# Kernel optimization log

Measured on AMD Instinct MI355X. Metric: run time of the kernel, lower is better.

## Reference

```python
import jax, jax.numpy as jnp
import numpy as np

LN_EPS = 1e-5
NORM_EPS = 1e-12


def channel_layernorm(x, w, b):
    # LayerNorm over channel dim of NCHW tensor (torch permutes to NHWC; equivalent)
    mu = x.mean(axis=1, keepdims=True)
    var = x.var(axis=1, keepdims=True)
    xn = (x - mu) / jnp.sqrt(var + LN_EPS)
    return xn * w[None, :, None, None] + b[None, :, None, None]


def pconv(x, w):
    # 1x1 pointwise conv, w: (out_ch, in_ch)
    return jnp.einsum('bchw,oc->bohw', x, w)


def dwconv3(x, w):
    # depthwise 3x3, padding 1; w: (ch, 1, 3, 3)
    return jax.lax.conv_general_dilated(
        x, w, window_strides=(1, 1), padding='SAME',
        feature_group_count=x.shape[1],
        dimension_numbers=('NCHW', 'OIHW', 'NCHW'))


def l2norm(x):
    n = jnp.sqrt(jnp.sum(x * x, axis=-1, keepdims=True))
    return x / jnp.maximum(n, NORM_EPS)


def setup_inputs() -> dict:
    key = jax.random.key(0)
    ks = jax.random.split(key, 8)
    B, C, H, W = 4, 128, 128, 128
    NH, G = 8, 2

    def w(k, shape, fan_in):
        return jax.random.normal(k, shape, dtype=jnp.float32) * (fan_in ** -0.5)

    return {
        'x': jax.random.normal(ks[0], (B, C, H, W), dtype=jnp.float32),
        'ln1_w': jnp.ones((C,), jnp.float32),
        'ln1_b': jnp.zeros((C,), jnp.float32),
        'temperature': jnp.ones((NH, 1, 1), jnp.float32),
        'qkv_p_w': w(ks[1], (3 * C, C), C),
        'qkv_d_w': w(ks[2], (3 * C, 1, 3, 3), 9),
        'proj_w': w(ks[3], (C, C), C),
        'ln2_w': jnp.ones((C,), jnp.float32),
        'ln2_b': jnp.zeros((C,), jnp.float32),
        'g1_w': w(ks[4], (2 * G * C, C), C),
        'gd_w': w(ks[5], (2 * G * C, 1, 3, 3), 9),
        'g2_w': w(ks[6], (C, G * C), G * C),
        'num_heads': NH,
    }


def reference(x, ln1_w, ln1_b, temperature, qkv_p_w, qkv_d_w, proj_w,
              ln2_w, ln2_b, g1_w, gd_w, g2_w, num_heads):
    b, c, h, w_ = x.shape
    d = c // num_heads

    # --- MDTA branch ---
    y = channel_layernorm(x, ln1_w, ln1_b)
    qkv = dwconv3(pconv(y, qkv_p_w), qkv_d_w)  # (b, 3c, h, w)
    q, k, v = jnp.split(qkv, 3, axis=1)
    q = l2norm(q.reshape(b, num_heads, d, h * w_))
    k = l2norm(k.reshape(b, num_heads, d, h * w_))
    v = v.reshape(b, num_heads, d, h * w_)
    # transposed (channel) attention: (b, heads, d, d)
    attn = jnp.einsum('bhdn,bhen->bhde', q, k) * temperature[None]
    attn = jax.nn.softmax(attn, axis=-1)
    out = jnp.einsum('bhde,bhen->bhdn', attn, v).reshape(b, c, h, w_)
    x = x + pconv(out, proj_w)

    # --- GDFN branch ---
    y = channel_layernorm(x, ln2_w, ln2_b)
    hdn = dwconv3(pconv(y, g1_w), gd_w)  # (b, 2*gamma*c, h, w)
    x1, x2 = jnp.split(hdn, 2, axis=1)
    g = jax.nn.gelu(x1, approximate=False) * x2
    x = x + pconv(g, g2_w)
    return x
```

## Files before the change

kernel.cpp:

```cpp
#include <hip/hip_runtime.h>
#include <cstdint>
#include <cstddef>

typedef float f32x4 __attribute__((ext_vector_type(4)));
typedef __bf16 bf16x8 __attribute__((ext_vector_type(8)));

__device__ __forceinline__ float b2f(unsigned short u) {
    union { unsigned int i; float f; } z; z.i = ((unsigned int)u) << 16; return z.f;
}
__device__ __forceinline__ unsigned short f2b(float f) {
    union { float f; unsigned int i; } z; z.f = f;
    unsigned int x = z.i;
    return (unsigned short)((x + 0x7FFFu + ((x >> 16) & 1u)) >> 16);
}

static constexpr int C = 128;
static constexpr int NP = 16384;
static constexpr int NH = 8;

struct Ptr11 { const float* p[11]; };
__constant__ int kWN[11]   = {128, 128, 8, 49152, 3456, 16384, 128, 128, 65536, 4608, 32768};
__constant__ int kWOff[11] = {0, 128, 256, 272, 49424, 52880, 69264, 69392, 69520, 135056, 139664};
static constexpr int kWTotal = 172432;

__global__ __launch_bounds__(256)
void cvt_w_kernel(Ptr11 P, unsigned short* __restrict__ dst)
{
    int seg = blockIdx.y;
    int n = kWN[seg];
    int i = blockIdx.x * 256 + threadIdx.x;
    if (i >= n) return;
    dst[kWOff[seg] + i] = f2b(P.p[seg][i]);
}

__device__ __forceinline__ void dw8(const unsigned short* base, int y, int xi,
                                    const float* wr, float* o)
{
    uint4 rv0 = uint4{0,0,0,0}, rv1, rv2 = uint4{0,0,0,0};
    if (y > 0)   rv0 = *(const uint4*)(base - 128);
    rv1 = *(const uint4*)(base);
    if (y < 127) rv2 = *(const uint4*)(base + 128);
    uint4 rows[3] = {rv0, rv1, rv2};
    #pragma unroll
    for (int j = 0; j < 8; ++j) o[j] = 0.f;
    #pragma unroll
    for (int r = 0; r < 3; ++r) {
        union { uint4 v; unsigned short u[8]; } cv; cv.v = rows[r];
        int lh = __shfl_up((int)cv.u[7], 1, 16);
        int rh = __shfl_down((int)cv.u[0], 1, 16);
        float p[10];
        p[0] = (xi > 0)   ? b2f((unsigned short)lh) : 0.f;
        p[9] = (xi < 120) ? b2f((unsigned short)rh) : 0.f;
        #pragma unroll
        for (int j = 0; j < 8; ++j) p[j + 1] = b2f(cv.u[j]);
        #pragma unroll
        for (int j = 0; j < 8; ++j)
            o[j] += wr[r * 3] * p[j] + wr[r * 3 + 1] * p[j + 1] + wr[r * 3 + 2] * p[j + 2];
    }
}

template <int COUT>
__device__ __forceinline__ void gemm_core_tr(
    const unsigned short* BsT,
    const unsigned short* __restrict__ W,
    unsigned short* __restrict__ OutB,
    int n0, int tid)
{
    const int lane = tid & 63;
    const int wid  = tid >> 6;
    const int ln16 = lane & 15, quad = lane >> 4;
    const int wy = wid >> 1, wx = wid & 1;
    const char* bs = (const char*)BsT;
    const int swz = (ln16 & 7) << 4;
    int rbase[4];
    #pragma unroll
    for (int nt = 0; nt < 4; ++nt) {
        int n = wx * 64 + nt * 16 + ln16;
        rbase[nt] = n * 256 + quad * 16;
    }

    for (int cc = 0; cc < COUT / 128; ++cc) {
        const int m0 = cc * 128;
        f32x4 acc[4][4];
        #pragma unroll
        for (int i = 0; i < 4; ++i)
            #pragma unroll
            for (int j = 0; j < 4; ++j) acc[i][j] = f32x4{0.f, 0.f, 0.f, 0.f};

        #pragma unroll
        for (int k0 = 0; k0 < 128; k0 += 32) {
            bf16x8 afr[4], bfr[4];
            #pragma unroll
            for (int mt = 0; mt < 4; ++mt) {
                int m = m0 + wy * 64 + mt * 16 + ln16;
                uint4 v = *(const uint4*)(W + (size_t)m * 128 + k0 + quad * 8);
                afr[mt] = *(bf16x8*)&v;
            }
            #pragma unroll
            for (int nt = 0; nt < 4; ++nt) {
                uint4 v = *(const uint4*)(bs + ((rbase[nt] + k0 * 2) ^ swz));
                bfr[nt] = *(bf16x8*)&v;
            }
            #pragma unroll
            for (int mt = 0; mt < 4; ++mt)
                #pragma unroll
                for (int nt = 0; nt < 4; ++nt)
                    acc[mt][nt] = __builtin_amdgcn_mfma_f32_16x16x32_bf16(
                        afr[mt], bfr[nt], acc[mt][nt], 0, 0, 0);
        }
        #pragma unroll
        for (int mt = 0; mt < 4; ++mt)
            #pragma unroll
            for (int nt = 0; nt < 4; ++nt) {
                int co0 = m0 + wy * 64 + mt * 16 + quad * 4;
                int n = n0 + wx * 64 + nt * 16 + ln16;
                #pragma unroll
                for (int r = 0; r < 4; ++r)
                    OutB[(size_t)(co0 + r) * NP + n] = f2b(acc[mt][nt][r]);
            }
    }
}

template <int COUT>
__global__ __launch_bounds__(256)
void lngemm_kernel(const float* __restrict__ x,
                   const unsigned short* __restrict__ lg,
                   const unsigned short* __restrict__ lb,
                   const unsigned short* __restrict__ W,
                   unsigned short* __restrict__ Out)
{
    __shared__ unsigned short BsT[128 * 128];
    __shared__ float Ssum[8][128], Ssq[8][128], Mu[128], Rs[128];
    const int tid = threadIdx.x;
    const int b = blockIdx.y;
    const int n0 = blockIdx.x * 128;
    const int pxg = tid & 31;
    const int cseg = tid >> 5;
    const float* xb = x + (size_t)b * C * NP + n0 + pxg * 4;

    f32x4 hv[16];
    f32x4 vs = f32x4{0.f, 0.f, 0.f, 0.f}, vq = f32x4{0.f, 0.f, 0.f, 0.f};
    #pragma unroll
    for (int i = 0; i < 16; ++i) {
        f32x4 v = *(const f32x4*)(xb + (size_t)(cseg * 16 + i) * NP);
        hv[i] = v; vs += v; vq += v * v;
    }
    #pragma unroll
    for (int j = 0; j < 4; ++j) {
        Ssum[cseg][pxg * 4 + j] = vs[j];
        Ssq[cseg][pxg * 4 + j]  = vq[j];
    }
    __syncthreads();
    if (tid < 128) {
        float s = 0.f, q = 0.f;
        #pragma unroll
        for (int e = 0; e < 8; ++e) { s += Ssum[e][tid]; q += Ssq[e][tid]; }
        float mu = s * (1.f / 128.f);
        float var = q * (1.f / 128.f) - mu * mu;
        Mu[tid] = mu;
        Rs[tid] = rsqrtf(fmaxf(var, 0.f) + 1e-5f);
    }
    __syncthreads();
    f32x4 mu4 = *(const f32x4*)(&Mu[pxg * 4]);
    f32x4 rs4 = *(const f32x4*)(&Rs[pxg * 4]);

    float gwv[16], bwv[16];
    #pragma unroll
    for (int i = 0; i < 16; ++i) {
        gwv[i] = b2f(lg[cseg * 16 + i]);
        bwv[i] = b2f(lb[cseg * 16 + i]);
    }

    char* p = (char*)BsT;
    #pragma unroll
    for (int j = 0; j < 4; ++j) {
        int n = pxg * 4 + j;
        union { uint4 v[2]; unsigned short u[16]; } o;
        #pragma unroll
        for (int i = 0; i < 16; ++i)
            o.u[i] = f2b((hv[i][j] - mu4[j]) * rs4[j] * gwv[i] + bwv[i]);
        int base = n * 256 + cseg * 32;
        int sw = (n & 7) << 4;
        *(uint4*)(p + (base ^ sw))        = o.v[0];
        *(uint4*)(p + ((base + 16) ^ sw)) = o.v[1];
    }
    __syncthreads();
    gemm_core_tr<COUT>(BsT, W, Out + (size_t)b * COUT * NP, n0, tid);
}

template <int COUT>
__global__ __launch_bounds__(256)
void gemm_bf16t_kernel(const unsigned short* __restrict__ W,
                       const unsigned short* __restrict__ Xt,
                       unsigned short* __restrict__ Out)
{
    __shared__ unsigned short BsT[128 * 128];
    const int tid = threadIdx.x;
    const int b = blockIdx.y;
    const int n0 = blockIdx.x * 128;
    const unsigned short* Xb = Xt + (size_t)b * NP * 128 + (size_t)n0 * 128;
    char* p = (char*)BsT;
    #pragma unroll
    for (int r = 0; r < 8; ++r) {
        int flat = tid + r * 256;
        int n = flat >> 4, ks = flat & 15;
        uint4 v = *(const uint4*)(Xb + (size_t)n * 128 + ks * 8);
        *(uint4*)(p + ((n * 256 + ks * 16) ^ ((n & 7) << 4))) = v;
    }
    __syncthreads();
    gemm_core_tr<COUT>(BsT, W, Out + (size_t)b * COUT * NP, n0, tid);
}

__global__ __launch_bounds__(256)
void dwv_kernel(const unsigned short* __restrict__ big,
                const unsigned short* __restrict__ w9,
                unsigned short* __restrict__ midv)
{
    int t = blockIdx.x * 256 + threadIdx.x;
    int xi = (t & 15) * 8;
    int y  = (t >> 4) & 127;
    int bc = t >> 11;
    int c  = bc & 127;
    int b  = bc >> 7;
    int ch = 256 + c;
    const unsigned short* base = big + ((size_t)b * 384 + ch) * NP + y * 128 + xi;

    float wr[9];
    #pragma unroll
    for (int i = 0; i < 9; ++i) wr[i] = b2f(w9[ch * 9 + i]);

    float o[8];
    dw8(base, y, xi, wr, o);

    union { uint4 v; unsigned short u[8]; } res;
    #pragma unroll
    for (int j = 0; j < 8; ++j) res.u[j] = f2b(o[j]);
    *(uint4*)(midv + (size_t)bc * NP + y * 128 + xi) = res.v;
}

__global__ __launch_bounds__(256)
void dwqkgram_kernel(const unsigned short* __restrict__ big,
                     const unsigned short* __restrict__ w9,
                     float* __restrict__ Spart,
                     float* __restrict__ Npart)
{
    __shared__ unsigned short qs_[16 * 520];
    __shared__ unsigned short ks_[16 * 520];
    __shared__ float Sred[4][256];
    const int h = blockIdx.x, b = blockIdx.y, sp = blockIdx.z;
    const int tid = threadIdx.x;
    const int wid = tid >> 6, lane = tid & 63;
    const int xi = (tid & 15) * 8;
    const int yr = (tid >> 4) & 3;
    const int y  = sp * 4 + yr;
    const int bh = b * NH + h;
    float* Np = Npart + ((size_t)bh * 32 + sp) * 32;

    #pragma unroll
    for (int p = 0; p < 4; ++p) {
        int qc = p * 4 + wid;
        #pragma unroll
        for (int s = 0; s < 2; ++s) {
            int ch = s * 128 + h * 16 + qc;
            const unsigned short* base = big + ((size_t)b * 384 + ch) * NP + y * 128 + xi;
            float wr[9];
            #pragma unroll
            for (int i = 0; i < 9; ++i) wr[i] = b2f(w9[ch * 9 + i]);
            float o[8];
            dw8(base, y, xi, wr, o);
            union { uint4 v; unsigned short u[8]; } res;
            float ss = 0.f;
            #pragma unroll
            for (int j = 0; j < 8; ++j) {
                res.u[j] = f2b(o[j]);
                float vv = b2f(res.u[j]);
                ss += vv * vv;
            }
            unsigned short* tile = s ? ks_ : qs_;
            *(uint4*)(&tile[qc * 520 + yr * 128 + xi]) = res.v;
            #pragma unroll
            for (int od = 32; od > 0; od >>= 1) ss += __shfl_xor(ss, od, 64);
            if (lane == 0) Np[s * 16 + qc] = ss;
        }
    }
    __syncthreads();

    const int ln16 = lane & 15, quad = lane >> 4;
    f32x4 acc = f32x4{0.f, 0.f, 0.f, 0.f};
    #pragma unroll
    for (int i = 0; i < 4; ++i) {
        int off = wid * 128 + i * 32 + quad * 8;
        uint4 qv = *(const uint4*)(&qs_[ln16 * 520 + off]);
        uint4 kv = *(const uint4*)(&ks_[ln16 * 520 + off]);
        acc = __builtin_amdgcn_mfma_f32_16x16x32_bf16(*(bf16x8*)&qv, *(bf16x8*)&kv, acc, 0, 0, 0);
    }
    #pragma unroll
    for (int r = 0; r < 4; ++r) Sred[wid][(quad * 4 + r) * 16 + ln16] = acc[r];
    __syncthreads();
    float ssum = Sred[0][tid] + Sred[1][tid] + Sred[2][tid] + Sred[3][tid];
    Spart[((size_t)bh * 32 + sp) * 256 + tid] = ssum;
}

__global__ __launch_bounds__(256)
void softwp_kernel(const float* __restrict__ Spart, const float* __restrict__ Npart,
                   const unsigned short* __restrict__ temp,
                   const unsigned short* __restrict__ proj,
                   unsigned short* __restrict__ W2)
{
    __shared__ float Ps[256];
    int bh = blockIdx.x;
    int b = bh >> 3, h = bh & 7;
    int t = threadIdx.x;
    int dq = t >> 4, dk = t & 15;
    float sacc = 0.f;
    const float* Sp = Spart + (size_t)bh * 32 * 256;
    #pragma unroll
    for (int j = 0; j < 32; ++j) sacc += Sp[j * 256 + t];
    const float* Np = Npart + (size_t)bh * 32 * 32;
    float sq = 0.f, sk = 0.f;
    #pragma unroll
    for (int sp = 0; sp < 32; ++sp) { sq += Np[sp * 32 + dq]; sk += Np[sp * 32 + 16 + dk]; }
    float nq = fmaxf(sqrtf(sq), 1e-12f);
    float nk = fmaxf(sqrtf(sk), 1e-12f);
    float v = sacc / (nq * nk) * b2f(temp[h]);
    float m = v;
    #pragma unroll
    for (int o = 8; o > 0; o >>= 1) m = fmaxf(m, __shfl_xor(m, o, 16));
    float e = __expf(v - m);
    float s = e;
    #pragma unroll
    for (int o = 8; o > 0; o >>= 1) s += __shfl_xor(s, o, 16);
    Ps[t] = e / s;
    __syncthreads();

    int co = t >> 1;
    int eo = (t & 1) * 8;
    union { uint4 v[2]; unsigned short u[16]; } pw;
    pw.v[0] = *(const uint4*)(proj + (size_t)co * 128 + h * 16);
    pw.v[1] = *(const uint4*)(proj + (size_t)co * 128 + h * 16 + 8);
    float prw[16];
    #pragma unroll
    for (int d = 0; d < 16; ++d) prw[d] = b2f(pw.u[d]);
    union { uint4 v; unsigned short u[8]; } o8;
    #pragma unroll
    for (int j = 0; j < 8; ++j) {
        int ee = eo + j;
        float s2 = 0.f;
        #pragma unroll
        for (int d = 0; d < 16; ++d) s2 += prw[d] * Ps[d * 16 + ee];
        o8.u[j] = f2b(s2);
    }
    *(uint4*)(W2 + ((size_t)b * 128 + co) * 128 + h * 16 + eo) = o8.v;
}

__global__ __launch_bounds__(256)
void projln_kernel(const unsigned short* __restrict__ W2,
                   const unsigned short* __restrict__ V,
                   const float* __restrict__ Res,
                   float* __restrict__ Xmid,
                   const unsigned short* __restrict__ lg,
                   const unsigned short* __restrict__ lb,
                   unsigned short* __restrict__ Y2t)
{
    __shared__ unsigned short Bs[128][130];
    __shared__ float RedS[2][128], RedQ[2][128], Mu[128], Rs[128];
    const int tid = threadIdx.x;
    const int b = blockIdx.y;
    const int n0 = blockIdx.x * 128;
    const unsigned short* Wb = W2 + (size_t)b * 16384;

    #pragma unroll
    for (int r = 0; r < 8; ++r) {
        int flat = tid + r * 256;
        int kk = flat >> 4, nn = (flat & 15) * 8;
        uint4 v = *(const uint4*)(V + ((size_t)b * 128 + kk) * NP + n0 + nn);
        unsigned int* d = (unsigned int*)&Bs[kk][nn];
        d[0] = v.x; d[1] = v.y; d[2] = v.z; d[3] = v.w;
    }
    __syncthreads();

    const int lane = tid & 63, wid = tid >> 6;
    const int ln16 = lane & 15, quad = lane >> 4;
    const int wy = wid >> 1, wx = wid & 1;

    f32x4 acc[4][4];
    #pragma unroll
    for (int i = 0; i < 4; ++i)
        #pragma unroll
        for (int j = 0; j < 4; ++j) acc[i][j] = f32x4{0.f, 0.f, 0.f, 0.f};

    #pragma unroll
    for (int k0 = 0; k0 < 128; k0 += 32) {
        bf16x8 afr[4], bfr[4];
        #pragma unroll
        for (int mt = 0; mt < 4; ++mt) {
            int m = wy * 64 + mt * 16 + ln16;
            uint4 v = *(const uint4*)(Wb + (size_t)m * 128 + k0 + quad * 8);
            afr[mt] = *(bf16x8*)&v;
        }
        #pragma unroll
        for (int nt = 0; nt < 4; ++nt) {
            int n = wx * 64 + nt * 16 + ln16;
            union { bf16x8 v; unsigned short u[8]; } tmp;
            #pragma unroll
            for (int j = 0; j < 8; ++j) tmp.u[j] = Bs[k0 + quad * 8 + j][n];
            bfr[nt] = tmp.v;
        }
        #pragma unroll
        for (int mt = 0; mt < 4; ++mt)
            #pragma unroll
            for (int nt = 0; nt < 4; ++nt)
                acc[mt][nt] = __builtin_amdgcn_mfma_f32_16x16x32_bf16(
                    afr[mt], bfr[nt], acc[mt][nt], 0, 0, 0);
    }

    size_t base = (size_t)b * 128 * NP;
    float ps[4] = {0.f, 0.f, 0.f, 0.f}, pq[4] = {0.f, 0.f, 0.f, 0.f};
    #pragma unroll
    for (int mt = 0; mt < 4; ++mt)
        #pragma unroll
        for (int nt = 0; nt < 4; ++nt) {
            int co0 = wy * 64 + mt * 16 + quad * 4;
            int n = n0 + wx * 64 + nt * 16 + ln16;
            #pragma unroll
            for (int r = 0; r < 4; ++r) {
                size_t idx = base + (size_t)(co0 + r) * NP + n;
                float tv = Res[idx] + acc[mt][nt][r];
                Xmid[idx] = tv;
                acc[mt][nt][r] = tv;
                ps[nt] += tv; pq[nt] += tv * tv;
            }
        }
    #pragma unroll
    for (int nt = 0; nt < 4; ++nt) {
        ps[nt] += __shfl_xor(ps[nt], 16, 64); ps[nt] += __shfl_xor(ps[nt], 32, 64);
        pq[nt] += __shfl_xor(pq[nt], 16, 64); pq[nt] += __shfl_xor(pq[nt], 32, 64);
    }
    if (quad == 0) {
        #pragma unroll
        for (int nt = 0; nt < 4; ++nt) {
            int nn = wx * 64 + nt * 16 + ln16;
            RedS[wy][nn] = ps[nt]; RedQ[wy][nn] = pq[nt];
        }
    }
    __syncthreads();
    if (tid < 128) {
        float s = RedS[0][tid] + RedS[1][tid];
        float q = RedQ[0][tid] + RedQ[1][tid];
        float mu = s * (1.f / 128.f);
        float var = q * (1.f / 128.f) - mu * mu;
        Mu[tid] = mu; Rs[tid] = rsqrtf(fmaxf(var, 0.f) + 1e-5f);
    }
    __syncthreads();

    char* p = (char*)Bs;
    #pragma unroll
    for (int mt = 0; mt < 4; ++mt) {
        int co0 = wy * 64 + mt * 16 + quad * 4;
        union { uint2 v; unsigned short u[4]; } gv, bv;
        gv.v = *(const uint2*)(lg + co0);
        bv.v = *(const uint2*)(lb + co0);
        float gw[4], bw[4];
        #pragma unroll
        for (int r = 0; r < 4; ++r) { gw[r] = b2f(gv.u[r]); bw[r] = b2f(bv.u[r]); }
        #pragma unroll
        for (int nt = 0; nt < 4; ++nt) {
            int nn = wx * 64 + nt * 16 + ln16;
            float mu = Mu[nn], rs = Rs[nn];
            union { uint2 v; unsigned short u[4]; } t2;
            #pragma unroll
            for (int r = 0; r < 4; ++r)
                t2.u[r] = f2b((acc[mt][nt][r] - mu) * rs * gw[r] + bw[r]);
            int addr = (nn * 256 + co0 * 2) ^ ((nn & 7) << 4);
            *(uint2*)(p + addr) = t2.v;
        }
    }
    __syncthreads();

    unsigned short* Yo = Y2t + (size_t)b * NP * 128 + (size_t)n0 * 128;
    #pragma unroll
    for (int r = 0; r < 8; ++r) {
        int flat = tid + r * 256;
        int n = flat >> 4, ks = flat & 15;
        uint4 v = *(const uint4*)(p + ((n * 256 + ks * 16) ^ ((n & 7) << 4)));
        *(uint4*)(Yo + (size_t)n * 128 + ks * 8) = v;
    }
}

template <int K, int EPI>
__global__ __launch_bounds__(256)
void gemm_pconv(const unsigned short* __restrict__ W,
                const unsigned short* __restrict__ X,
                void* __restrict__ Out,
                const float* __restrict__ Res,
                int Cout)
{
    __shared__ unsigned short Bs[32][130];
    const int tid = threadIdx.x;
    const int b = blockIdx.z;
    const int n0 = blockIdx.x * 128;
    const int m0 = blockIdx.y * 128;
    const unsigned short* Xb = X + (size_t)b * K * NP;
    const int wid = tid >> 6;
    const int lane = tid & 63;
    const int ln16 = lane & 15;
    const int quad = lane >> 4;
    const int wy = wid >> 1;
    const int wx = wid & 1;

    f32x4 acc[4][4];
    #pragma unroll
    for (int i = 0; i < 4; ++i)
        #pragma unroll
        for (int j = 0; j < 4; ++j)
            acc[i][j] = f32x4{0.f, 0.f, 0.f, 0.f};

    for (int k0 = 0; k0 < K; k0 += 32) {
        #pragma unroll
        for (int r = 0; r < 2; ++r) {
            int flat = tid + r * 256;
            int kk = flat >> 4;
            int nn = (flat & 15) * 8;
            uint4 v = *(const uint4*)(Xb + (size_t)(k0 + kk) * NP + n0 + nn);
            unsigned int* d = (unsigned int*)&Bs[kk][nn];
            d[0] = v.x; d[1] = v.y; d[2] = v.z; d[3] = v.w;
        }
        __syncthreads();

        bf16x8 afr[4];
        #pragma unroll
        for (int mt = 0; mt < 4; ++mt) {
            int m = m0 + wy * 64 + mt * 16 + ln16;
            uint4 v = *(const uint4*)(W + (size_t)m * K + k0 + quad * 8);
            afr[mt] = *(bf16x8*)&v;
        }
        bf16x8 bfr[4];
        #pragma unroll
        for (int nt = 0; nt < 4; ++nt) {
            int n = wx * 64 + nt * 16 + ln16;
            union { bf16x8 v; unsigned short u[8]; } tmp;
            #pragma unroll
            for (int j = 0; j < 8; ++j) tmp.u[j] = Bs[quad * 8 + j][n];
            bfr[nt] = tmp.v;
        }
        #pragma unroll
        for (int mt = 0; mt < 4; ++mt)
            #pragma unroll
            for (int nt = 0; nt < 4; ++nt)
                acc[mt][nt] = __builtin_amdgcn_mfma_f32_16x16x32_bf16(
                    afr[mt], bfr[nt], acc[mt][nt], 0, 0, 0);
        __syncthreads();
    }

    size_t outbase = (size_t)b * Cout * NP;
    #pragma unroll
    for (int mt = 0; mt < 4; ++mt) {
        #pragma unroll
        for (int nt = 0; nt < 4; ++nt) {
            int co0 = m0 + wy * 64 + mt * 16 + quad * 4;
            int n = n0 + wx * 64 + nt * 16 + ln16;
            #pragma unroll
            for (int r = 0; r < 4; ++r) {
                float v = acc[mt][nt][r];
                size_t idx = outbase + (size_t)(co0 + r) * NP + n;
                if (EPI == 0) ((unsigned short*)Out)[idx] = f2b(v);
                else          ((float*)Out)[idx] = Res[idx] + v;
            }
        }
    }
}

__global__ __launch_bounds__(256)
void dwgelu_kernel(const unsigned short* __restrict__ hdn,
                   const unsigned short* __restrict__ w9,
                   unsigned short* __restrict__ g)
{
    int t = blockIdx.x * 256 + threadIdx.x;
    int xi = (t & 15) * 8;
    int y  = (t >> 4) & 127;
    int bc = t >> 11;
    int c  = bc & 255;
    int b  = bc >> 8;
    const unsigned short* base1 = hdn + ((size_t)b * 512 + c) * NP + y * 128 + xi;
    const unsigned short* base2 = base1 + (size_t)256 * NP;

    float w1[9], w2[9];
    #pragma unroll
    for (int i = 0; i < 9; ++i) {
        w1[i] = b2f(w9[c * 9 + i]);
        w2[i] = b2f(w9[(c + 256) * 9 + i]);
    }

    float a1[8], a2[8];
    dw8(base1, y, xi, w1, a1);
    dw8(base2, y, xi, w2, a2);

    union { uint4 v; unsigned short u[8]; } res;
    #pragma unroll
    for (int j = 0; j < 8; ++j) {
        float u = a1[j];
        float tt = u * (0.7978845608f + 0.0356774081f * u * u);
        float e = __expf(2.f * tt);
        float th = 1.f - 2.f / (e + 1.f);
        float ge = 0.5f * u * (1.f + th);
        res.u[j] = f2b(ge * a2[j]);
    }
    *(uint4*)(g + (size_t)bc * NP + y * 128 + xi) = res.v;
}

struct Bufs {
    float* xmid;
    unsigned short* y2;
    unsigned short* big;
    unsigned short* mid;
    float* Spart;
    float* Npart;
    unsigned short* W2;
};

static void run_pipeline(const float* x_f32, float* out_f32,
                         const unsigned short* w,
                         const Bufs& B, int nb, hipStream_t stream)
{
    const unsigned short* ln1_w   = w + 0;
    const unsigned short* ln1_b   = w + 128;
    const unsigned short* temp    = w + 256;
    const unsigned short* qkv_p_w = w + 272;
    const unsigned short* qkv_d_w = w + 49424;
    const unsigned short* proj_w  = w + 52880;
    const unsigned short* ln2_w   = w + 69264;
    const unsigned short* ln2_b   = w + 69392;
    const unsigned short* g1_w    = w + 69520;
    const unsigned short* gd_w    = w + 135056;
    const unsigned short* g2_w    = w + 139664;

    lngemm_kernel<384><<<dim3(NP / 128, nb), 256, 0, stream>>>(x_f32, ln1_w, ln1_b, qkv_p_w, B.big);
    dwqkgram_kernel<<<dim3(NH, nb, 32), 256, 0, stream>>>(B.big, qkv_d_w, B.Spart, B.Npart);
    dwv_kernel<<<nb * 128 * NP / 2048, 256, 0, stream>>>(B.big, qkv_d_w, B.mid);
    softwp_kernel<<<nb * NH, 256, 0, stream>>>(B.Spart, B.Npart, temp, proj_w, B.W2);
    projln_kernel<<<dim3(NP / 128, nb), 256, 0, stream>>>(B.W2, B.mid, x_f32, B.xmid, ln2_w, ln2_b, B.y2);

    gemm_bf16t_kernel<512><<<dim3(NP / 128, nb), 256, 0, stream>>>(g1_w, B.y2, B.big);
    dwgelu_kernel<<<nb * 256 * NP / 2048, 256, 0, stream>>>(B.big, gd_w, B.mid);
    gemm_pconv<256, 1><<<dim3(NP / 128, 1, nb), 256, 0, stream>>>(g2_w, B.mid, out_f32, B.xmid, 128);
}

extern "C" void kernel_launch(void* const* d_in, const int* in_sizes, int n_in,
                              void* d_out, int out_size, void* d_ws, size_t ws_size,
                              hipStream_t stream)
{
    (void)in_sizes; (void)n_in; (void)out_size;
    const float* x = (const float*)d_in[0];
    char* ws = (char*)d_ws;

    size_t off = 0;
    unsigned short* wpack = (unsigned short*)(ws + off);
    off += (size_t)kWTotal * 2;
    off = (off + 255) & ~(size_t)255;
    size_t header = off;

    auto layout = [&](int nb, size_t o, Bufs& B) -> size_t {
        B.xmid = (float*)(ws + o);           o += (size_t)nb * C * NP * 4;
        B.y2   = (unsigned short*)(ws + o);  o += (size_t)nb * C * NP * 2;
        B.big  = (unsigned short*)(ws + o);  o += (size_t)nb * 512 * NP * 2;
        B.mid  = (unsigned short*)(ws + o);  o += (size_t)nb * 256 * NP * 2;
        B.Spart = (float*)(ws + o);          o += (size_t)nb * NH * 32 * 256 * 4;
        B.Npart = (float*)(ws + o);          o += (size_t)nb * NH * 32 * 32 * 4;
        B.W2   = (unsigned short*)(ws + o);  o += (size_t)nb * 128 * 128 * 2;
        return o;
    };

    Ptr11 P;
    for (int i = 0; i < 11; ++i) P.p[i] = (const float*)d_in[i + 1];
    cvt_w_kernel<<<dim3(256, 11), 256, 0, stream>>>(P, wpack);

    Bufs Bfull;
    size_t need_full = layout(4, header, Bfull);

    if (ws_size >= need_full) {
        run_pipeline(x, (float*)d_out, wpack, Bfull, 4, stream);
    } else {
        Bufs B1;
        layout(1, header, B1);
        for (int b = 0; b < 4; ++b) {
            run_pipeline(x + (size_t)b * C * NP,
                         (float*)d_out + (size_t)b * C * NP,
                         wpack, B1, 1, stream);
        }
    }
}
```

Before: 253.0 us.

## Fuse V depthwise conv into projln and store residual midpoint in bf16

Removes the standalone dwv kernel. The V-channel depthwise 3x3 convolution is now computed directly inside projln_kernel, which writes it straight into shared memory instead of round-tripping through the mid buffer. The intermediate residual xmid is also stored as bf16 instead of fp32, halving its write and later read in the final pconv. This saves one launch and several full-tensor memory passes, at the cost of extra loads per block from neighbouring rows and reduced precision on the residual path.

```diff
diff --git a/kernel.cpp b/kernel.cpp
--- a/kernel.cpp
+++ b/kernel.cpp
@@ -209,33 +209,6 @@
     }
     __syncthreads();
     gemm_core_tr<COUT>(BsT, W, Out + (size_t)b * COUT * NP, n0, tid);
-}
-
-__global__ __launch_bounds__(256)
-void dwv_kernel(const unsigned short* __restrict__ big,
-                const unsigned short* __restrict__ w9,
-                unsigned short* __restrict__ midv)
-{
-    int t = blockIdx.x * 256 + threadIdx.x;
-    int xi = (t & 15) * 8;
-    int y  = (t >> 4) & 127;
-    int bc = t >> 11;
-    int c  = bc & 127;
-    int b  = bc >> 7;
-    int ch = 256 + c;
-    const unsigned short* base = big + ((size_t)b * 384 + ch) * NP + y * 128 + xi;
-
-    float wr[9];
-    #pragma unroll
-    for (int i = 0; i < 9; ++i) wr[i] = b2f(w9[ch * 9 + i]);
-
-    float o[8];
-    dw8(base, y, xi, wr, o);
-
-    union { uint4 v; unsigned short u[8]; } res;
-    #pragma unroll
-    for (int j = 0; j < 8; ++j) res.u[j] = f2b(o[j]);
-    *(uint4*)(midv + (size_t)bc * NP + y * 128 + xi) = res.v;
 }
 
 __global__ __launch_bounds__(256)
@@ -355,9 +328,10 @@
 
 __global__ __launch_bounds__(256)
 void projln_kernel(const unsigned short* __restrict__ W2,
-                   const unsigned short* __restrict__ V,
+                   const unsigned short* __restrict__ big,
+                   const unsigned short* __restrict__ w9,
                    const float* __restrict__ Res,
-                   float* __restrict__ Xmid,
+                   unsigned short* __restrict__ Xmid,
                    const unsigned short* __restrict__ lg,
                    const unsigned short* __restrict__ lb,
                    unsigned short* __restrict__ Y2t)
@@ -366,16 +340,29 @@
     __shared__ float RedS[2][128], RedQ[2][128], Mu[128], Rs[128];
     const int tid = threadIdx.x;
     const int b = blockIdx.y;
-    const int n0 = blockIdx.x * 128;
+    const int y = blockIdx.x;
+    const int n0 = y * 128;
     const unsigned short* Wb = W2 + (size_t)b * 16384;
 
-    #pragma unroll
-    for (int r = 0; r < 8; ++r) {
-        int flat = tid + r * 256;
-        int kk = flat >> 4, nn = (flat & 15) * 8;
-        uint4 v = *(const uint4*)(V + ((size_t)b * 128 + kk) * NP + n0 + nn);
-        unsigned int* d = (unsigned int*)&Bs[kk][nn];
-        d[0] = v.x; d[1] = v.y; d[2] = v.z; d[3] = v.w;
+    {
+        const int xi = (tid & 15) * 8;
+        const int crow = tid >> 4;
+        #pragma unroll
+        for (int p = 0; p < 8; ++p) {
+            int c = p * 16 + crow;
+            int ch = 256 + c;
+            const unsigned short* base = big + ((size_t)b * 384 + ch) * NP + n0 + xi;
+            float wr[9];
+            #pragma unroll
+            for (int i = 0; i < 9; ++i) wr[i] = b2f(w9[ch * 9 + i]);
+            float o[8];
+            dw8(base, y, xi, wr, o);
+            union { uint4 v; unsigned int d[4]; unsigned short u[8]; } res;
+            #pragma unroll
+            for (int j = 0; j < 8; ++j) res.u[j] = f2b(o[j]);
+            unsigned int* d = (unsigned int*)&Bs[c][xi];
+            d[0] = res.d[0]; d[1] = res.d[1]; d[2] = res.d[2]; d[3] = res.d[3];
+        }
     }
     __syncthreads();
 
@@ -426,7 +413,7 @@
             for (int r = 0; r < 4; ++r) {
                 size_t idx = base + (size_t)(co0 + r) * NP + n;
                 float tv = Res[idx] + acc[mt][nt][r];
-                Xmid[idx] = tv;
+                Xmid[idx] = f2b(tv);
                 acc[mt][nt][r] = tv;
                 ps[nt] += tv; pq[nt] += tv * tv;
             }
@@ -487,12 +474,12 @@
     }
 }
 
-template <int K, int EPI>
+template <int K>
 __global__ __launch_bounds__(256)
 void gemm_pconv(const unsigned short* __restrict__ W,
                 const unsigned short* __restrict__ X,
-                void* __restrict__ Out,
-                const float* __restrict__ Res,
+                float* __restrict__ Out,
+                const unsigned short* __restrict__ Res,
                 int Cout)
 {
     __shared__ unsigned short Bs[32][130];
@@ -561,10 +548,8 @@
             int n = n0 + wx * 64 + nt * 16 + ln16;
             #pragma unroll
             for (int r = 0; r < 4; ++r) {
-                float v = acc[mt][nt][r];
                 size_t idx = outbase + (size_t)(co0 + r) * NP + n;
-                if (EPI == 0) ((unsigned short*)Out)[idx] = f2b(v);
-                else          ((float*)Out)[idx] = Res[idx] + v;
+                Out[idx] = b2f(Res[idx]) + acc[mt][nt][r];
             }
         }
     }
@@ -609,7 +594,7 @@
 }
 
 struct Bufs {
-    float* xmid;
+    unsigned short* xmid;
     unsigned short* y2;
     unsigned short* big;
     unsigned short* mid;
@@ -636,13 +621,13 @@
 
     lngemm_kernel<384><<<dim3(NP / 128, nb), 256, 0, stream>>>(x_f32, ln1_w, ln1_b, qkv_p_w, B.big);
     dwqkgram_kernel<<<dim3(NH, nb, 32), 256, 0, stream>>>(B.big, qkv_d_w, B.Spart, B.Npart);
-    dwv_kernel<<<nb * 128 * NP / 2048, 256, 0, stream>>>(B.big, qkv_d_w, B.mid);
     softwp_kernel<<<nb * NH, 256, 0, stream>>>(B.Spart, B.Npart, temp, proj_w, B.W2);
-    projln_kernel<<<dim3(NP / 128, nb), 256, 0, stream>>>(B.W2, B.mid, x_f32, B.xmid, ln2_w, ln2_b, B.y2);
+    projln_kernel<<<dim3(NP / 128, nb), 256, 0, stream>>>(B.W2, B.big, qkv_d_w, x_f32,
+                                                          B.xmid, ln2_w, ln2_b, B.y2);
 
     gemm_bf16t_kernel<512><<<dim3(NP / 128, nb), 256, 0, stream>>>(g1_w, B.y2, B.big);
     dwgelu_kernel<<<nb * 256 * NP / 2048, 256, 0, stream>>>(B.big, gd_w, B.mid);
-    gemm_pconv<256, 1><<<dim3(NP / 128, 1, nb), 256, 0, stream>>>(g2_w, B.mid, out_f32, B.xmid, 128);
+    gemm_pconv<256><<<dim3(NP / 128, 1, nb), 256, 0, stream>>>(g2_w, B.mid, out_f32, B.xmid, 128);
 }
 
 extern "C" void kernel_launch(void* const* d_in, const int* in_sizes, int n_in,
@@ -660,7 +645,7 @@
     size_t header = off;
 
     auto layout = [&](int nb, size_t o, Bufs& B) -> size_t {
-        B.xmid = (float*)(ws + o);           o += (size_t)nb * C * NP * 4;
+        B.xmid = (unsigned short*)(ws + o);  o += (size_t)nb * C * NP * 2;
         B.y2   = (unsigned short*)(ws + o);  o += (size_t)nb * C * NP * 2;
         B.big  = (unsigned short*)(ws + o);  o += (size_t)nb * 512 * NP * 2;
         B.mid  = (unsigned short*)(ws + o);  o += (size_t)nb * 256 * NP * 2;
```

Measured after the change: 248.6 us. Within noise of the previous version (-1.8%).
